# Kernel optimization log

Hardware: AMD Instinct MI355X
Metric: run time of the kernel (lower is better)

Reference implementation:

```python
import jax, jax.numpy as jnp
import numpy as np

B, S, D, H = 4, 1024, 512, 8
DH = D // H  # 64 head dim; max_len == S for the masked (preceding_only) skew path


def setup_inputs() -> dict:
    key = jax.random.key(0)
    ks = jax.random.split(key, 8)
    queries = jax.random.normal(ks[0], (B, S, D), jnp.float32)
    keys_ = jax.random.normal(ks[1], (B, S, D), jnp.float32)
    values = jax.random.normal(ks[2], (B, S, D), jnp.float32)
    Wq = jax.random.normal(ks[3], (D, D), jnp.float32) * 0.03
    Wk = jax.random.normal(ks[4], (D, D), jnp.float32) * 0.03
    Wv = jax.random.normal(ks[5], (D, D), jnp.float32) * 0.03
    Wo = jax.random.normal(ks[6], (D, D), jnp.float32) * 0.03
    rel_emb = jax.random.normal(ks[7], (H, DH, S), jnp.float32) * 0.03  # preceding_only -> len == max_len
    i = jnp.arange(S)
    mask = jnp.where(i[None, :] > i[:, None], -1e9, 0.0).astype(jnp.float32)[None, None]  # [1,1,S,S] causal
    return {"queries": queries, "keys": keys_, "values": values, "mask": mask,
            "Wq": Wq, "Wk": Wk, "Wv": Wv, "Wo": Wo, "rel_emb": rel_emb}


def _skewed_rel_bias(q, rel_emb):
    # q: [B,H,S,DH], rel_emb: [H,DH,L] with L == max_len == S
    b, h, s, _ = q.shape
    L = rel_emb.shape[-1]
    qe = jnp.einsum('bhsd,hdl->bhsl', q, rel_emb)  # [B,H,S,L]
    # _qe_masking: keep qe[..., i, j] where j >= L-1-i
    lengths = (L - 1) - jnp.arange(s)
    keep = (jnp.arange(L)[None, :] >= lengths[:, None]).astype(qe.dtype)
    qe = qe * keep
    # skew: pad one column on the left, fold into [B,H,L+1,S], drop first row
    qe = jnp.pad(qe, ((0, 0), (0, 0), (0, 0), (1, 0)))
    qe = qe.reshape(b, h, L + 1, s)[:, :, 1:, :]  # [B,H,L,S]
    return qe


def reference(queries, keys, values, mask, Wq, Wk, Wv, Wo, rel_emb):
    b, s, _ = queries.shape
    h, dh, _ = rel_emb.shape
    scale = dh ** -0.5

    def split(x):  # [B,S,H*DH] -> [B,H,S,DH]
        return x.reshape(b, s, h, dh).transpose(0, 2, 1, 3)

    q = split(queries @ Wq)
    k = split(keys @ Wk)
    v = split(values @ Wv)

    logits = jnp.einsum('bhsd,bhtd->bhst', q, k)
    logits = logits + _skewed_rel_bias(q, rel_emb)
    logits = (logits + mask[:, :, :s, :s]) * scale  # original scales after adding mask
    weights = jax.nn.softmax(logits, axis=-1)
    ctx = jnp.einsum('bhst,bhtd->bhsd', weights, v)
    ctx = ctx.transpose(0, 2, 1, 3).reshape(b, s, h * dh)
    return ctx @ Wo
```

## Files before the change

kernel.cpp:

```cpp
#include <hip/hip_runtime.h>
#include <hip/hip_bf16.h>

#define SB 4
#define SS 1024
#define SD 512
#define SH 8
#define SDH 64

typedef short bf16x8 __attribute__((ext_vector_type(8)));
typedef float f32x4 __attribute__((ext_vector_type(4)));

#define MFMA(a, b, c) __builtin_amdgcn_mfma_f32_16x16x32_bf16(a, b, c, 0, 0, 0)

__device__ __forceinline__ void load_lds16(const void* g, void* l) {
  __builtin_amdgcn_global_load_lds(
      (__attribute__((address_space(1))) void*)(const_cast<void*>(g)),
      (__attribute__((address_space(3))) void*)(l), 16, 0, 0);
}

__global__ __launch_bounds__(256) void k_prep(
    const float* __restrict__ q, const float* __restrict__ k, const float* __restrict__ v,
    const float* __restrict__ Wq, const float* __restrict__ Wk, const float* __restrict__ Wv,
    const float* __restrict__ Wo, const float* __restrict__ rel,
    __hip_bfloat16* __restrict__ Xq, __hip_bfloat16* __restrict__ Xk,
    __hip_bfloat16* __restrict__ Xv, __hip_bfloat16* __restrict__ Wqt,
    __hip_bfloat16* __restrict__ Wkt, __hip_bfloat16* __restrict__ Wvt,
    __hip_bfloat16* __restrict__ Wot, __hip_bfloat16* __restrict__ relT) {
  __shared__ float tile[32][33];
  const int y = blockIdx.y, x = blockIdx.x, t = threadIdx.x;
  if (y < 3) {
    const float2* in = (const float2*)(y == 0 ? q : y == 1 ? k : v);
    __hip_bfloat162* out = (__hip_bfloat162*)(y == 0 ? Xq : y == 1 ? Xk : Xv);
    const int n2 = SB * SS * SD / 2;
    int i = x * 256 + t, st = 512 * 256;
    for (; i < n2; i += st) out[i] = __float22bfloat162_rn(in[i]);
    return;
  }
  int tx = t & 31, ty = t >> 5;
  if (y < 5) {
    int which = (y - 3) * 2 + (x >> 8), idx = x & 255;
    const float* ip = which == 0 ? Wq : which == 1 ? Wk : which == 2 ? Wv : Wo;
    __hip_bfloat16* op = which == 0 ? Wqt : which == 1 ? Wkt : which == 2 ? Wvt : Wot;
    int c0 = (idx & 15) * 32, r0 = (idx >> 4) * 32;
    for (int rr = ty; rr < 32; rr += 8) tile[rr][tx] = ip[(size_t)(r0 + rr) * SD + c0 + tx];
    __syncthreads();
    for (int cc = ty; cc < 32; cc += 8)
      op[(size_t)(c0 + cc) * SD + r0 + tx] = __float2bfloat16(tile[tx][cc]);
    return;
  }
  int hd = x >> 6, idx = x & 63;
  int c0 = (idx >> 1) * 32, r0 = (idx & 1) * 32;
  const float* ip = rel + (size_t)hd * SDH * SS;
  __hip_bfloat16* op = relT + (size_t)hd * SDH * SS;
  for (int rr = ty; rr < 32; rr += 8) tile[rr][tx] = ip[(size_t)(r0 + rr) * SS + c0 + tx];
  __syncthreads();
  for (int cc = ty; cc < 32; cc += 8)
    op[(size_t)(c0 + cc) * SDH + r0 + tx] = __float2bfloat16(tile[tx][cc]);
}

__device__ __forceinline__ void gemm_core(const __hip_bfloat16* __restrict__ A,
                                          const __hip_bfloat16* __restrict__ Bt,
                                          void* __restrict__ Cout, int mode) {
  __shared__ __hip_bfloat16 As[128 * 64];
  __shared__ __hip_bfloat16 Bs[64 * 64];
  const int t = threadIdx.x, w = t >> 6, lane = t & 63;
  const int quad = lane >> 4, l16 = lane & 15;
  const int m0 = blockIdx.y * 128, n0 = blockIdx.x * 64;
  const int wm = (w >> 1) * 64, wn = (w & 1) * 32;
  f32x4 zero4 = {0.0f, 0.0f, 0.0f, 0.0f};
  f32x4 acc[4][2];
#pragma unroll
  for (int mi = 0; mi < 4; ++mi)
#pragma unroll
    for (int nj = 0; nj < 2; ++nj) acc[mi][nj] = zero4;

  for (int kt = 0; kt < SD; kt += 64) {
#pragma unroll
    for (int c = 0; c < 4; ++c) {
      int ofs = c * 256 + t;
      int row = ofs >> 3, col = (ofs & 7) ^ (row & 7);
      load_lds16(A + (size_t)(m0 + row) * SD + kt + col * 8,
                 (char*)As + (size_t)(c * 256 + w * 64) * 16);
    }
#pragma unroll
    for (int c = 0; c < 2; ++c) {
      int ofs = c * 256 + t;
      int row = ofs >> 3, col = (ofs & 7) ^ (row & 7);
      load_lds16(Bt + (size_t)(n0 + row) * SD + kt + col * 8,
                 (char*)Bs + (size_t)(c * 256 + w * 64) * 16);
    }
    __syncthreads();
    bf16x8 af[4][2], bfr[2][2];
#pragma unroll
    for (int mi = 0; mi < 4; ++mi) {
      int row = wm + mi * 16 + l16;
#pragma unroll
      for (int ks = 0; ks < 2; ++ks)
        af[mi][ks] = *(const bf16x8*)((const char*)As + row * 128 +
                                      ((ks * 4 + quad) ^ (row & 7)) * 16);
    }
#pragma unroll
    for (int nj = 0; nj < 2; ++nj) {
      int row = wn + nj * 16 + l16;
#pragma unroll
      for (int ks = 0; ks < 2; ++ks)
        bfr[nj][ks] = *(const bf16x8*)((const char*)Bs + row * 128 +
                                       ((ks * 4 + quad) ^ (row & 7)) * 16);
    }
#pragma unroll
    for (int mi = 0; mi < 4; ++mi)
#pragma unroll
      for (int nj = 0; nj < 2; ++nj) {
        acc[mi][nj] = MFMA(af[mi][0], bfr[nj][0], acc[mi][nj]);
        acc[mi][nj] = MFMA(af[mi][1], bfr[nj][1], acc[mi][nj]);
      }
    __syncthreads();
  }
#pragma unroll
  for (int mi = 0; mi < 4; ++mi)
#pragma unroll
    for (int nj = 0; nj < 2; ++nj)
#pragma unroll
      for (int r = 0; r < 4; ++r) {
        int m = m0 + wm + mi * 16 + quad * 4 + r;
        int n = n0 + wn + nj * 16 + l16;
        float v = acc[mi][nj][r];
        if (mode == 2) {
          ((float*)Cout)[(size_t)m * SD + n] = v;
        } else {
          int b = m >> 10, s = m & 1023, hh = n >> 6, dh = n & 63;
          __hip_bfloat16 bv = __float2bfloat16(v);
          if (mode == 0)
            ((__hip_bfloat16*)Cout)[((size_t)(b * SH + hh) * SS + s) * SDH + dh] = bv;
          else
            ((__hip_bfloat16*)Cout)[((size_t)(b * SH + hh) * SDH + dh) * SS + s] = bv;
        }
      }
}

__global__ __launch_bounds__(256) void k_gemm_qkv(
    const __hip_bfloat16* __restrict__ Xq, const __hip_bfloat16* __restrict__ Xk,
    const __hip_bfloat16* __restrict__ Xv, const __hip_bfloat16* __restrict__ Wqt,
    const __hip_bfloat16* __restrict__ Wkt, const __hip_bfloat16* __restrict__ Wvt,
    __hip_bfloat16* __restrict__ Qb, __hip_bfloat16* __restrict__ Kb,
    __hip_bfloat16* __restrict__ Vt) {
  int z = blockIdx.z;
  const __hip_bfloat16* A = z == 0 ? Xq : z == 1 ? Xk : Xv;
  const __hip_bfloat16* Bt = z == 0 ? Wqt : z == 1 ? Wkt : Wvt;
  void* C = z == 0 ? (void*)Qb : z == 1 ? (void*)Kb : (void*)Vt;
  gemm_core(A, Bt, C, z == 2 ? 1 : 0);
}

__global__ __launch_bounds__(256) void k_gemm_o(const __hip_bfloat16* __restrict__ CTX,
                                                const __hip_bfloat16* __restrict__ Wot,
                                                float* __restrict__ Out) {
  gemm_core(CTX, Wot, Out, 2);
}

__global__ __launch_bounds__(256) void k_flash(const __hip_bfloat16* __restrict__ Qb,
                                               const __hip_bfloat16* __restrict__ Kb,
                                               const __hip_bfloat16* __restrict__ Vt,
                                               const __hip_bfloat16* __restrict__ relT,
                                               float* __restrict__ Opart,
                                               float* __restrict__ lpart,
                                               __hip_bfloat16* __restrict__ CTX) {
  __shared__ __hip_bfloat16 Klds[64 * 64];
  __shared__ __hip_bfloat16 Vlds[64 * 64];
  __shared__ __hip_bfloat16 REs[128 * 64];
  __shared__ __hip_bfloat16 QEP[64 * 136];
  const int t = threadIdx.x, w = t >> 6, lane = t & 63;
  const int quad = lane >> 4, l16 = lane & 15;
  const int idx = blockIdx.x, bh = blockIdx.y, h = bh & 7;
  int tI, c, jt0, nt;
  bool single;
  if (idx < 8) {
    tI = idx; c = 0; jt0 = 0; nt = tI + 1; single = true;
  } else {
    tI = 8 + ((idx - 8) >> 1); c = (idx - 8) & 1;
    jt0 = c ? 8 : 0; nt = c ? (tI - 7) : 8; single = false;
  }
  const int i0 = tI * 64;
  const size_t qbase = (size_t)bh * SS * SDH;
  const __hip_bfloat16* Rp = relT + (size_t)h * SS * SDH;

  const int qrow = i0 + w * 16 + l16;
  bf16x8 qf0 = *(const bf16x8*)(Qb + qbase + (size_t)qrow * SDH + quad * 8);
  bf16x8 qf1 = *(const bf16x8*)(Qb + qbase + (size_t)qrow * SDH + 32 + quad * 8);

  f32x4 zero4 = {0.0f, 0.0f, 0.0f, 0.0f};
  f32x4 acc_o[4];
#pragma unroll
  for (int dt = 0; dt < 4; ++dt) acc_o[dt] = zero4;
  float ls[4] = {0.0f, 0.0f, 0.0f, 0.0f};
  const int rloc = quad * 4;
  __hip_bfloat16* myrow = QEP + (size_t)(w * 16 + rloc) * 136;

  for (int jt = 0; jt < nt; ++jt) {
    const int jtile = jt0 + jt, j0 = jtile * 64;
    const int l0 = 960 - 64 * (tI - jtile);
#pragma unroll
    for (int cc = 0; cc < 2; ++cc) {
      int ofs = cc * 256 + t;
      int row = ofs >> 3, col = (ofs & 7) ^ (row & 7);
      load_lds16(Kb + qbase + (size_t)(j0 + row) * SDH + col * 8,
                 (char*)Klds + (size_t)(cc * 256 + w * 64) * 16);
      load_lds16(Vt + (size_t)bh * SDH * SS + (size_t)row * SS + j0 + col * 8,
                 (char*)Vlds + (size_t)(cc * 256 + w * 64) * 16);
    }
#pragma unroll
    for (int cc = 0; cc < 4; ++cc) {
      int ofs = cc * 256 + t;
      int row = ofs >> 3, col = (ofs & 7) ^ (row & 7);
      int lr = l0 + row;
      if (lr > 1023) lr = 1023;
      load_lds16(Rp + (size_t)lr * SDH + col * 8,
                 (char*)REs + (size_t)(cc * 256 + w * 64) * 16);
    }
    __syncthreads();

    f32x4 s[4];
#pragma unroll
    for (int nj = 0; nj < 4; ++nj) {
      int row = nj * 16 + l16;
      bf16x8 b0 = *(const bf16x8*)((const char*)Klds + row * 128 + (quad ^ (row & 7)) * 16);
      bf16x8 b1 = *(const bf16x8*)((const char*)Klds + row * 128 + ((4 + quad) ^ (row & 7)) * 16);
      f32x4 z = zero4;
      z = MFMA(qf0, b0, z);
      z = MFMA(qf1, b1, z);
      s[nj] = z;
    }
#pragma unroll
    for (int nc = 0; nc < 8; ++nc) {
      int row = nc * 16 + l16;
      bf16x8 b0 = *(const bf16x8*)((const char*)REs + row * 128 + (quad ^ (row & 7)) * 16);
      bf16x8 b1 = *(const bf16x8*)((const char*)REs + row * 128 + ((4 + quad) ^ (row & 7)) * 16);
      f32x4 e = zero4;
      e = MFMA(qf0, b0, e);
      e = MFMA(qf1, b1, e);
#pragma unroll
      for (int r = 0; r < 4; ++r)
        myrow[r * 136 + nc * 16 + l16] = __float2bfloat16(e[r]);
    }

#pragma unroll
    for (int nj = 0; nj < 4; ++nj) {
      int jc = nj * 16 + l16, jcol = j0 + jc;
#pragma unroll
      for (int r = 0; r < 4; ++r) {
        int irow = i0 + w * 16 + rloc + r;
        float bias = __bfloat162float(myrow[r * 136 + 63 + jc - (rloc + r)]);
        float val = (s[nj][r] + bias) * 0.125f - 8.0f;
        float p = (jcol <= irow) ? __expf(val) : 0.0f;
        s[nj][r] = p;
        ls[r] += p;
      }
    }
#pragma unroll
    for (int nj = 0; nj < 4; ++nj)
#pragma unroll
      for (int r = 0; r < 4; ++r)
        myrow[r * 136 + nj * 16 + l16] = __float2bfloat16(s[nj][r]);

#pragma unroll
    for (int js = 0; js < 2; ++js) {
      bf16x8 pa = *(const bf16x8*)(QEP + (size_t)(w * 16 + l16) * 136 + js * 32 + quad * 8);
#pragma unroll
      for (int dt = 0; dt < 4; ++dt) {
        int row = dt * 16 + l16;
        bf16x8 vb = *(const bf16x8*)((const char*)Vlds + row * 128 +
                                     ((js * 4 + quad) ^ (row & 7)) * 16);
        acc_o[dt] = MFMA(pa, vb, acc_o[dt]);
      }
    }
    __syncthreads();
  }
  float rsum[4];
#pragma unroll
  for (int r = 0; r < 4; ++r) {
    float sum = ls[r];
    sum += __shfl_xor(sum, 1, 64);
    sum += __shfl_xor(sum, 2, 64);
    sum += __shfl_xor(sum, 4, 64);
    sum += __shfl_xor(sum, 8, 64);
    rsum[r] = sum;
  }
  if (single) {
    const int b = bh >> 3;
#pragma unroll
    for (int r = 0; r < 4; ++r) {
      int row = w * 16 + rloc + r;
      float rl = 1.0f / rsum[r];
#pragma unroll
      for (int dt = 0; dt < 4; ++dt)
        CTX[((size_t)b * SS + i0 + row) * SD + h * SDH + dt * 16 + l16] =
            __float2bfloat16(acc_o[dt][r] * rl);
    }
  } else {
    const size_t pbase = ((size_t)bh * 8 + (tI - 8)) * 2 + c;
    float* Op = Opart + pbase * 4096;
#pragma unroll
    for (int r = 0; r < 4; ++r) {
      int row = w * 16 + rloc + r;
#pragma unroll
      for (int dt = 0; dt < 4; ++dt) Op[row * 64 + dt * 16 + l16] = acc_o[dt][r];
      if (l16 == 0) lpart[pbase * 64 + row] = rsum[r];
    }
  }
}

__global__ __launch_bounds__(256) void k_reduce2(const float* __restrict__ Opart,
                                                 const float* __restrict__ lpart,
                                                 __hip_bfloat16* __restrict__ CTX) {
  const int bx = blockIdx.x, bh = blockIdx.y, b = bh >> 3, h = bh & 7;
  const int tI = 8 + bx, tid = threadIdx.x;
  __shared__ float lsum[64];
  const size_t base = ((size_t)bh * 8 + bx) * 2;
  if (tid < 64) lsum[tid] = lpart[base * 64 + tid] + lpart[(base + 1) * 64 + tid];
  __syncthreads();
  const int e0 = tid * 16, row = e0 >> 6, d0 = e0 & 63;
  const float4* p0 = (const float4*)(Opart + base * 4096);
  const float4* p1 = (const float4*)(Opart + (base + 1) * 4096);
  const float rl = 1.0f / lsum[row];
  __hip_bfloat16* op = CTX + ((size_t)b * SS + tI * 64 + row) * SD + h * SDH + d0;
#pragma unroll
  for (int vv = 0; vv < 4; ++vv) {
    float4 x = p0[tid * 4 + vv], y = p1[tid * 4 + vv];
    op[vv * 4 + 0] = __float2bfloat16((x.x + y.x) * rl);
    op[vv * 4 + 1] = __float2bfloat16((x.y + y.y) * rl);
    op[vv * 4 + 2] = __float2bfloat16((x.z + y.z) * rl);
    op[vv * 4 + 3] = __float2bfloat16((x.w + y.w) * rl);
  }
}

extern "C" void kernel_launch(void* const* d_in, const int* in_sizes, int n_in,
                              void* d_out, int out_size, void* d_ws, size_t ws_size,
                              hipStream_t stream) {
  const float* queries = (const float*)d_in[0];
  const float* keys    = (const float*)d_in[1];
  const float* values  = (const float*)d_in[2];
  const float* Wq = (const float*)d_in[4];
  const float* Wk = (const float*)d_in[5];
  const float* Wv = (const float*)d_in[6];
  const float* Wo = (const float*)d_in[7];
  const float* rel = (const float*)d_in[8];

  char* ws = (char*)d_ws;
  size_t off = 0;
  auto alloc = [&](size_t bytes) {
    char* p = ws + off;
    off += (bytes + 255) & ~(size_t)255;
    return p;
  };
  const size_t XB = (size_t)SB * SS * SD * 2;
  const size_t WB = (size_t)SD * SD * 2;
  __hip_bfloat16* Wqt  = (__hip_bfloat16*)alloc(WB);
  __hip_bfloat16* Wkt  = (__hip_bfloat16*)alloc(WB);
  __hip_bfloat16* Wvt  = (__hip_bfloat16*)alloc(WB);
  __hip_bfloat16* Wot  = (__hip_bfloat16*)alloc(WB);
  __hip_bfloat16* relT = (__hip_bfloat16*)alloc((size_t)SH * SS * SDH * 2);
  __hip_bfloat16* Qb   = (__hip_bfloat16*)alloc(XB);
  __hip_bfloat16* Kb   = (__hip_bfloat16*)alloc(XB);
  __hip_bfloat16* Vt   = (__hip_bfloat16*)alloc(XB);
  __hip_bfloat16* CTX  = (__hip_bfloat16*)alloc(XB);
  char* uni = alloc(3 * XB);
  __hip_bfloat16* Xq = (__hip_bfloat16*)uni;
  __hip_bfloat16* Xk = (__hip_bfloat16*)(uni + XB);
  __hip_bfloat16* Xv = (__hip_bfloat16*)(uni + 2 * XB);
  float* Opart = (float*)uni;
  float* lpart = (float*)(uni + (size_t)32 * 8 * 2 * 4096 * 4);
  if (off > ws_size) return;

  k_prep<<<dim3(512, 6), dim3(256), 0, stream>>>(
      queries, keys, values, Wq, Wk, Wv, Wo, rel,
      Xq, Xk, Xv, Wqt, Wkt, Wvt, Wot, relT);
  k_gemm_qkv<<<dim3(SD / 64, SB * SS / 128, 3), dim3(256), 0, stream>>>(
      Xq, Xk, Xv, Wqt, Wkt, Wvt, Qb, Kb, Vt);
  k_flash<<<dim3(24, SB * SH), dim3(256), 0, stream>>>(Qb, Kb, Vt, relT, Opart, lpart, CTX);
  k_reduce2<<<dim3(8, SB * SH), dim3(256), 0, stream>>>(Opart, lpart, CTX);
  k_gemm_o<<<dim3(SD / 64, SB * SS / 128), dim3(256), 0, stream>>>(CTX, Wot, (float*)d_out);
}
```

Before: 158.0 us.

## Widen GEMM tiles to 128x128 and reuse rel-emb half across flash iterations

The projection GEMMs now use 128x128 output tiles per block instead of 128x64, so each block reuses its A tile across twice as many columns, at the cost of more accumulator registers and half as many blocks. In the flash kernel, the 128-row relative-embedding window slides by 64 rows per key tile, so the code now keeps the two halves in a ping-pong LDS buffer. Each step loads and multiplies only the new 64-row half, and the full window is computed only on the first iteration. This roughly halves the rel-bias MFMA work and LDS loads, but adds phase-indexed addressing and relies on the QEP row buffer keeping the previous half valid between iterations.

```diff
diff --git a/kernel.cpp b/kernel.cpp
--- a/kernel.cpp
+++ b/kernel.cpp
@@ -62,17 +62,17 @@
                                           const __hip_bfloat16* __restrict__ Bt,
                                           void* __restrict__ Cout, int mode) {
   __shared__ __hip_bfloat16 As[128 * 64];
-  __shared__ __hip_bfloat16 Bs[64 * 64];
+  __shared__ __hip_bfloat16 Bs[128 * 64];
   const int t = threadIdx.x, w = t >> 6, lane = t & 63;
   const int quad = lane >> 4, l16 = lane & 15;
-  const int m0 = blockIdx.y * 128, n0 = blockIdx.x * 64;
-  const int wm = (w >> 1) * 64, wn = (w & 1) * 32;
+  const int m0 = blockIdx.y * 128, n0 = blockIdx.x * 128;
+  const int wm = (w >> 1) * 64, wn = (w & 1) * 64;
   f32x4 zero4 = {0.0f, 0.0f, 0.0f, 0.0f};
-  f32x4 acc[4][2];
+  f32x4 acc[4][4];
 #pragma unroll
   for (int mi = 0; mi < 4; ++mi)
 #pragma unroll
-    for (int nj = 0; nj < 2; ++nj) acc[mi][nj] = zero4;
+    for (int nj = 0; nj < 4; ++nj) acc[mi][nj] = zero4;
 
   for (int kt = 0; kt < SD; kt += 64) {
 #pragma unroll
@@ -81,16 +81,11 @@
       int row = ofs >> 3, col = (ofs & 7) ^ (row & 7);
       load_lds16(A + (size_t)(m0 + row) * SD + kt + col * 8,
                  (char*)As + (size_t)(c * 256 + w * 64) * 16);
-    }
-#pragma unroll
-    for (int c = 0; c < 2; ++c) {
-      int ofs = c * 256 + t;
-      int row = ofs >> 3, col = (ofs & 7) ^ (row & 7);
       load_lds16(Bt + (size_t)(n0 + row) * SD + kt + col * 8,
                  (char*)Bs + (size_t)(c * 256 + w * 64) * 16);
     }
     __syncthreads();
-    bf16x8 af[4][2], bfr[2][2];
+    bf16x8 af[4][2], bfr[4][2];
 #pragma unroll
     for (int mi = 0; mi < 4; ++mi) {
       int row = wm + mi * 16 + l16;
@@ -100,7 +95,7 @@
                                       ((ks * 4 + quad) ^ (row & 7)) * 16);
     }
 #pragma unroll
-    for (int nj = 0; nj < 2; ++nj) {
+    for (int nj = 0; nj < 4; ++nj) {
       int row = wn + nj * 16 + l16;
 #pragma unroll
       for (int ks = 0; ks < 2; ++ks)
@@ -110,7 +105,7 @@
 #pragma unroll
     for (int mi = 0; mi < 4; ++mi)
 #pragma unroll
-      for (int nj = 0; nj < 2; ++nj) {
+      for (int nj = 0; nj < 4; ++nj) {
         acc[mi][nj] = MFMA(af[mi][0], bfr[nj][0], acc[mi][nj]);
         acc[mi][nj] = MFMA(af[mi][1], bfr[nj][1], acc[mi][nj]);
       }
@@ -119,7 +114,7 @@
 #pragma unroll
   for (int mi = 0; mi < 4; ++mi)
 #pragma unroll
-    for (int nj = 0; nj < 2; ++nj)
+    for (int nj = 0; nj < 4; ++nj)
 #pragma unroll
       for (int r = 0; r < 4; ++r) {
         int m = m0 + wm + mi * 16 + quad * 4 + r;
@@ -198,6 +193,9 @@
   for (int jt = 0; jt < nt; ++jt) {
     const int jtile = jt0 + jt, j0 = jtile * 64;
     const int l0 = 960 - 64 * (tI - jtile);
+    const int m64 = l0 >> 6;
+    const int ph_lo = m64 & 1, ph_hi = 1 - ph_lo;
+    const bool first = (jt == 0);
 #pragma unroll
     for (int cc = 0; cc < 2; ++cc) {
       int ofs = cc * 256 + t;
@@ -208,13 +206,23 @@
                  (char*)Vlds + (size_t)(cc * 256 + w * 64) * 16);
     }
 #pragma unroll
-    for (int cc = 0; cc < 4; ++cc) {
+    for (int cc = 0; cc < 2; ++cc) {
       int ofs = cc * 256 + t;
       int row = ofs >> 3, col = (ofs & 7) ^ (row & 7);
-      int lr = l0 + row;
+      int lr = l0 + 64 + row;
       if (lr > 1023) lr = 1023;
       load_lds16(Rp + (size_t)lr * SDH + col * 8,
-                 (char*)REs + (size_t)(cc * 256 + w * 64) * 16);
+                 (char*)REs + ph_hi * 8192 + (size_t)(cc * 256 + w * 64) * 16);
+    }
+    if (first) {
+#pragma unroll
+      for (int cc = 0; cc < 2; ++cc) {
+        int ofs = cc * 256 + t;
+        int row = ofs >> 3, col = (ofs & 7) ^ (row & 7);
+        int lr = l0 + row;
+        load_lds16(Rp + (size_t)lr * SDH + col * 8,
+                   (char*)REs + ph_lo * 8192 + (size_t)(cc * 256 + w * 64) * 16);
+      }
     }
     __syncthreads();
 
@@ -231,15 +239,17 @@
     }
 #pragma unroll
     for (int nc = 0; nc < 8; ++nc) {
-      int row = nc * 16 + l16;
-      bf16x8 b0 = *(const bf16x8*)((const char*)REs + row * 128 + (quad ^ (row & 7)) * 16);
-      bf16x8 b1 = *(const bf16x8*)((const char*)REs + row * 128 + ((4 + quad) ^ (row & 7)) * 16);
+      if (nc < 4 && !first) continue;
+      int ph = (m64 + (nc >> 2)) & 1;
+      int prow = ph * 64 + (nc & 3) * 16 + l16;
+      bf16x8 b0 = *(const bf16x8*)((const char*)REs + prow * 128 + ((quad ^ (prow & 7))) * 16);
+      bf16x8 b1 = *(const bf16x8*)((const char*)REs + prow * 128 + (((4 + quad) ^ (prow & 7))) * 16);
       f32x4 e = zero4;
       e = MFMA(qf0, b0, e);
       e = MFMA(qf1, b1, e);
 #pragma unroll
       for (int r = 0; r < 4; ++r)
-        myrow[r * 136 + nc * 16 + l16] = __float2bfloat16(e[r]);
+        myrow[r * 136 + ph * 64 + (nc & 3) * 16 + l16] = __float2bfloat16(e[r]);
     }
 
 #pragma unroll
@@ -248,22 +258,26 @@
 #pragma unroll
       for (int r = 0; r < 4; ++r) {
         int irow = i0 + w * 16 + rloc + r;
-        float bias = __bfloat162float(myrow[r * 136 + 63 + jc - (rloc + r)]);
+        int off = 63 + jc - (rloc + r);
+        int pcol = ((m64 + (off >> 6)) & 1) * 64 + (off & 63);
+        float bias = __bfloat162float(myrow[r * 136 + pcol]);
         float val = (s[nj][r] + bias) * 0.125f - 8.0f;
         float p = (jcol <= irow) ? __expf(val) : 0.0f;
         s[nj][r] = p;
         ls[r] += p;
       }
     }
+    const int pc = ph_lo * 64;
 #pragma unroll
     for (int nj = 0; nj < 4; ++nj)
 #pragma unroll
       for (int r = 0; r < 4; ++r)
-        myrow[r * 136 + nj * 16 + l16] = __float2bfloat16(s[nj][r]);
+        myrow[r * 136 + pc + nj * 16 + l16] = __float2bfloat16(s[nj][r]);
 
 #pragma unroll
     for (int js = 0; js < 2; ++js) {
-      bf16x8 pa = *(const bf16x8*)(QEP + (size_t)(w * 16 + l16) * 136 + js * 32 + quad * 8);
+      bf16x8 pa = *(const bf16x8*)(QEP + (size_t)(w * 16 + l16) * 136 + pc +
+                                   js * 32 + quad * 8);
 #pragma unroll
       for (int dt = 0; dt < 4; ++dt) {
         int row = dt * 16 + l16;
@@ -373,9 +387,9 @@
   k_prep<<<dim3(512, 6), dim3(256), 0, stream>>>(
       queries, keys, values, Wq, Wk, Wv, Wo, rel,
       Xq, Xk, Xv, Wqt, Wkt, Wvt, Wot, relT);
-  k_gemm_qkv<<<dim3(SD / 64, SB * SS / 128, 3), dim3(256), 0, stream>>>(
+  k_gemm_qkv<<<dim3(SD / 128, SB * SS / 128, 3), dim3(256), 0, stream>>>(
       Xq, Xk, Xv, Wqt, Wkt, Wvt, Qb, Kb, Vt);
   k_flash<<<dim3(24, SB * SH), dim3(256), 0, stream>>>(Qb, Kb, Vt, relT, Opart, lpart, CTX);
   k_reduce2<<<dim3(8, SB * SH), dim3(256), 0, stream>>>(Opart, lpart, CTX);
-  k_gemm_o<<<dim3(SD / 64, SB * SS / 128), dim3(256), 0, stream>>>(CTX, Wot, (float*)d_out);
-}
+  k_gemm_o<<<dim3(SD / 128, SB * SS / 128), dim3(256), 0, stream>>>(CTX, Wot, (float*)d_out);
+}
```

Measured after the change: 154.1 us. 2.5% less time.
